# Optimization experiments

Hardware: AMD Instinct MI355X
Metric: run time of the kernel (lower is better)

Reference implementation:

```python
import jax, jax.numpy as jnp
import numpy as np

B, N, DIM, H, DH = 2, 1024, 1024, 16, 64
ROT = 32          # rotary dims (applied to first ROT channels of q,k,v)
NUM_MEM = 2       # learned memory kv
TOPK = 64         # sparse topk
QK_SCALE = 10.0   # qk_norm_scale
MASK_VAL = -jnp.finfo(jnp.float32).max


def rotate_half(x):
    # '... (2 d) -> ... 2 d', then cat(-x2, x1)
    x = x.reshape(*x.shape[:-1], 2, x.shape[-1] // 2)
    x1, x2 = x[..., 0, :], x[..., 1, :]
    return jnp.concatenate((-x2, x1), axis=-1)


def apply_rotary(t, freqs):
    # t: [b,h,n,rot], freqs: [n,rot]
    f = freqs[-t.shape[-2]:, :]
    return t * jnp.cos(f) + rotate_half(t) * jnp.sin(f)


def l2norm(t, eps=1e-12):
    n = jnp.sqrt(jnp.sum(t * t, axis=-1, keepdims=True))
    return t / jnp.maximum(n, eps)


def setup_inputs() -> dict:
    key = jax.random.key(0)
    ks = jax.random.split(key, 10)
    s = 0.02
    return {
        'x': jax.random.normal(ks[0], (B, N, DIM), jnp.float32),
        'rotary_pos_emb': jax.random.uniform(ks[1], (N, ROT), jnp.float32),
        'Wq': jax.random.normal(ks[2], (DIM, H * DH), jnp.float32) * s,
        'Wk': jax.random.normal(ks[3], (DIM, H * DH), jnp.float32) * s,
        'Wv': jax.random.normal(ks[4], (DIM, H * DH), jnp.float32) * s,
        'Wo': jax.random.normal(ks[5], (H * DH, DIM), jnp.float32) * s,
        'mem_k': jax.random.normal(ks[6], (H, NUM_MEM, DH), jnp.float32),
        'mem_v': jax.random.normal(ks[7], (H, NUM_MEM, DH), jnp.float32),
        'th_pre': jax.random.normal(ks[8], (H, H), jnp.float32) * (1.0 / H),
        'th_post': jax.random.normal(ks[9], (H, H), jnp.float32) * (1.0 / H),
    }


def reference(x, rotary_pos_emb, Wq, Wk, Wv, Wo, mem_k, mem_v, th_pre, th_post):
    b, n, _ = x.shape
    # projections -> [b,h,n,d]
    def split_heads(t):
        return t.reshape(b, n, H, DH).transpose(0, 2, 1, 3)
    q = split_heads(x @ Wq)
    k = split_heads(x @ Wk)
    v = split_heads(x @ Wv)
    # rotary on first ROT channels of q, k AND v (faithful to source)
    def rot(t):
        return jnp.concatenate(
            (apply_rotary(t[..., :ROT], rotary_pos_emb), t[..., ROT:]), axis=-1)
    q, k, v = rot(q), rot(k), rot(v)
    # memory key/values prepended along j
    mk = jnp.broadcast_to(mem_k[None], (b, H, NUM_MEM, DH))
    mv = jnp.broadcast_to(mem_v[None], (b, H, NUM_MEM, DH))
    k = jnp.concatenate((mk, k), axis=2)
    v = jnp.concatenate((mv, v), axis=2)
    # qk l2 norm (groups=1) and fixed scale
    q, k = l2norm(q), l2norm(k)
    dots = jnp.einsum('bhid,bhjd->bhij', q, k) * QK_SCALE  # [b,h,n,n+mem]
    pre_softmax_attn = dots
    # pre-softmax talking heads (1x1 conv over head dim)
    dots = jnp.einsum('hg,bgij->bhij', th_pre, dots)
    # causal mask (mem kv always visible: mask padded False on left)
    j = n + NUM_MEM
    i_idx = jnp.arange(n)[:, None]
    j_idx = jnp.arange(j)[None, :]
    causal = (j_idx - NUM_MEM) > i_idx
    dots = jnp.where(causal[None, None], MASK_VAL, dots)
    # sparse topk pruning
    top, _ = jax.lax.top_k(dots, TOPK)
    vk = top[..., -1:]
    dots = jnp.where(dots < vk, MASK_VAL, dots)
    attn = jax.nn.softmax(dots, axis=-1)
    post_softmax_attn = attn
    # post-softmax talking heads
    attn = jnp.einsum('hg,bgij->bhij', th_post, attn)
    out = jnp.einsum('bhij,bhjd->bhid', attn, v)
    out = out.transpose(0, 2, 1, 3).reshape(b, n, H * DH)
    out = out @ Wo
    return out, pre_softmax_attn, post_softmax_attn
```

## Files before the change

### kernel.cpp

```cpp
#include <hip/hip_runtime.h>
#include <stdint.h>

#define HN 16
#define DHD 64
#define NSEQ 1024
#define JCOL 1026
#define JP 1056
#define JP2 1088
#define ROTD 32
#define MASKV -3.402823466e+38f

typedef unsigned short ushort_t;
typedef __attribute__((ext_vector_type(8))) short short8;
typedef __attribute__((ext_vector_type(4))) short short4v;
typedef __attribute__((ext_vector_type(4))) float f32x4;
typedef __attribute__((ext_vector_type(2))) float f32x2;

__device__ inline ushort_t f2b(float f){ union{float f; unsigned int i;} v; v.f=f; unsigned x=v.i;
  return (ushort_t)((x + 0x7FFFu + ((x>>16)&1u))>>16); }

__device__ inline void gld16(const void* g, void* l){
  __builtin_amdgcn_global_load_lds((const __attribute__((address_space(1))) void*)g,
                                   (__attribute__((address_space(3))) void*)l, 16, 0, 0);
}

__device__ inline unsigned key_of(float f){
  unsigned u = __float_as_uint(f);
  return (u & 0x80000000u) ? ~u : (u | 0x80000000u);
}
__device__ inline float val_of(unsigned k){
  unsigned u = (k & 0x80000000u) ? (k & 0x7FFFFFFFu) : ~k;
  return __uint_as_float(u);
}

__global__ void k_zero(uint4* p, int n4){
  int i = blockIdx.x*blockDim.x + threadIdx.x;
  if (i < n4) p[i] = make_uint4(0u,0u,0u,0u);
}

__global__ __launch_bounds__(256) void k_x2b(const float4* __restrict__ x, ushort_t* __restrict__ xb){
  int i = blockIdx.x*blockDim.x + threadIdx.x;
  float4 v = x[i];
  ushort_t* d = xb + (size_t)i*4;
  d[0]=f2b(v.x); d[1]=f2b(v.y); d[2]=f2b(v.z); d[3]=f2b(v.w);
}

__global__ __launch_bounds__(256) void k_transpose(const float* w0, const float* w1,
                                                   const float* w2, const float* w3,
                                                   ushort_t* outw){
  const float* src = blockIdx.z==0?w0: blockIdx.z==1?w1: blockIdx.z==2?w2: w3;
  ushort_t* dst = outw + (size_t)blockIdx.z*1024*1024;
  __shared__ float t[64][65];
  int tid = threadIdx.x;
  int bx = blockIdx.x*64, by = blockIdx.y*64;
  #pragma unroll
  for (int p=0;p<16;p++){
    int idx = tid + p*256; int r = idx>>6, c = idx&63;
    t[r][c] = src[(size_t)(by + r)*1024 + bx + c];
  }
  __syncthreads();
  #pragma unroll
  for (int p=0;p<16;p++){
    int idx = tid + p*256; int a = idx>>6, c2 = idx&63;
    dst[(size_t)(bx + a)*1024 + by + c2] = f2b(t[c2][a]);
  }
}

__global__ __launch_bounds__(256) void k_qkv(const ushort_t* __restrict__ xb,
                                             const ushort_t* __restrict__ wt,
                                             const float* __restrict__ rpe,
                                             ushort_t* __restrict__ Qn,
                                             ushort_t* __restrict__ Kn,
                                             ushort_t* __restrict__ Vt){
  __shared__ __attribute__((aligned(16))) ushort_t As[64*32];
  __shared__ __attribute__((aligned(16))) ushort_t Bs[64*32];
  int tid = threadIdx.x;
  int m0 = blockIdx.x*64;
  int nt = blockIdx.y;
  const ushort_t* wsel = wt + (size_t)(nt>>4)*1024*1024;
  int c0 = (nt&15)*64;
  int w = tid>>6, lane = tid&63, n15 = lane&15, quad = lane>>4;
  int r = tid>>2, seg = tid&3;
  f32x4 acc[4];
  #pragma unroll
  for (int t=0;t<4;t++) acc[t] = (f32x4){0.f,0.f,0.f,0.f};
  for (int k0=0;k0<1024;k0+=32){
    __syncthreads();
    gld16(xb   + (size_t)(m0 + r)*1024 + k0 + seg*8, (void*)(As + tid*8));
    gld16(wsel + (size_t)(c0 + r)*1024 + k0 + seg*8, (void*)(Bs + tid*8));
    __builtin_amdgcn_s_waitcnt(0);
    __syncthreads();
    short8 a = *(const short8*)(As + (w*16 + n15)*32 + quad*8);
    #pragma unroll
    for (int t=0;t<4;t++){
      short8 b = *(const short8*)(Bs + (t*16 + n15)*32 + quad*8);
      acc[t] = __builtin_amdgcn_mfma_f32_16x16x32_bf16(a, b, acc[t], 0,0,0);
    }
  }
  int which = nt >> 4, h = nt & 15;
  int rowbase = m0 + w*16 + quad*4;
  int b = rowbase >> 10;
  float val[4][4];
  #pragma unroll
  for (int rr=0; rr<4; rr++){
    int n = (rowbase + rr) & 1023;
    float f0 = rpe[n*ROTD + n15];
    float f1 = rpe[n*ROTD + 16 + n15];
    float c0r = __cosf(f0), s0r = __sinf(f0);
    float c1r = __cosf(f1), s1r = __sinf(f1);
    val[0][rr] = acc[0][rr]*c0r - acc[1][rr]*s0r;
    val[1][rr] = acc[1][rr]*c1r + acc[0][rr]*s1r;
    val[2][rr] = acc[2][rr];
    val[3][rr] = acc[3][rr];
  }
  if (which < 2){
    #pragma unroll
    for (int rr=0; rr<4; rr++){
      float ss = val[0][rr]*val[0][rr] + val[1][rr]*val[1][rr]
               + val[2][rr]*val[2][rr] + val[3][rr]*val[3][rr];
      #pragma unroll
      for (int off=1; off<16; off<<=1) ss += __shfl_xor(ss, off);
      float sc = 1.f / fmaxf(sqrtf(ss), 1e-12f);
      int n = (rowbase + rr) & 1023;
      if (which == 0){
        ushort_t* dst = Qn + ((size_t)(b*16+h)*NSEQ + n)*64;
        #pragma unroll
        for (int t=0;t<4;t++) dst[t*16 + n15] = f2b(val[t][rr]*sc);
      } else {
        ushort_t* dst = Kn + ((size_t)(b*16+h)*JP2 + (n+2))*64;
        #pragma unroll
        for (int t=0;t<4;t++) dst[t*16 + n15] = f2b(val[t][rr]*sc);
      }
    }
  } else {
    #pragma unroll
    for (int rr=0; rr<4; rr++){
      int n = (rowbase + rr) & 1023;
      #pragma unroll
      for (int t=0;t<4;t++){
        int d = t*16 + n15;
        Vt[((size_t)(b*16+h)*64 + d)*JP + (n+2)] = f2b(val[t][rr]);
      }
    }
  }
}

__global__ void k_mem(const float* __restrict__ mem_k, const float* __restrict__ mem_v,
                      ushort_t* __restrict__ Kn, ushort_t* __restrict__ Vt){
  int tid = threadIdx.x;
  int d = tid & 63;
  int sub = tid >> 6;
  for (int p=0; p<8; p++){
    int pp = p*4 + sub; int h = pp >> 1, m = pp & 1;
    float kv = mem_k[(h*2+m)*64 + d];
    float ss = kv*kv;
    #pragma unroll
    for (int off=1; off<64; off<<=1) ss += __shfl_xor(ss, off);
    float sc = 1.f/fmaxf(sqrtf(ss), 1e-12f);
    ushort_t kb = f2b(kv*sc);
    ushort_t vb = f2b(mem_v[(h*2+m)*64 + d]);
    for (int b=0;b<2;b++){
      Kn[((size_t)(b*16+h)*JP2 + m)*64 + d] = kb;
      Vt[((size_t)(b*16+h)*64 + d)*JP + m] = vb;
    }
  }
}

__global__ __launch_bounds__(256) void k_dots(const ushort_t* __restrict__ Qn,
        const ushort_t* __restrict__ Kn, float* __restrict__ pre){
  __shared__ __attribute__((aligned(16))) ushort_t As[64*64];
  __shared__ __attribute__((aligned(16))) ushort_t Bs[64*64];
  int tid = threadIdx.x;
  int m0 = blockIdx.x*64;
  int n0 = blockIdx.y*64;
  int bh = blockIdx.z;
  const ushort_t* A  = Qn + (size_t)bh*NSEQ*64 + (size_t)m0*64;
  const ushort_t* Bb = Kn + (size_t)bh*JP2*64 + (size_t)n0*64;
  int w = tid>>6, lane = tid&63, n15 = lane&15, quad = lane>>4;
  gld16(A  + tid*8,        (void*)(As + tid*8));
  gld16(A  + 2048 + tid*8, (void*)(As + 2048 + tid*8));
  gld16(Bb + tid*8,        (void*)(Bs + tid*8));
  gld16(Bb + 2048 + tid*8, (void*)(Bs + 2048 + tid*8));
  __builtin_amdgcn_s_waitcnt(0);
  __syncthreads();
  f32x4 acc[4];
  #pragma unroll
  for (int t=0;t<4;t++) acc[t] = (f32x4){0.f,0.f,0.f,0.f};
  #pragma unroll
  for (int kq=0;kq<2;kq++){
    short8 a = *(const short8*)(As + (w*16+n15)*64 + kq*32 + quad*8);
    #pragma unroll
    for (int t=0;t<4;t++){
      short8 b = *(const short8*)(Bs + (t*16+n15)*64 + kq*32 + quad*8);
      acc[t] = __builtin_amdgcn_mfma_f32_16x16x32_bf16(a, b, acc[t], 0,0,0);
    }
  }
  int rowbase = m0 + w*16 + quad*4;
  #pragma unroll
  for (int t=0;t<4;t++){
    #pragma unroll
    for (int rr=0;rr<4;rr++){
      int col = n0 + t*16 + n15;
      if (col < JCOL)
        pre[((size_t)bh*NSEQ + rowbase+rr)*JCOL + col] = acc[t][rr]*10.f;
    }
  }
}

__global__ __launch_bounds__(1024, 8) void k_mixsoft(const float* __restrict__ pre,
        float* __restrict__ post, ushort_t* __restrict__ AM,
        const float* __restrict__ th_pre, const float* __restrict__ th_post){
  constexpr int NCH = 5;
  __shared__ __attribute__((aligned(16))) float S[16*1280];
  int tid  = threadIdx.x;
  int lane = tid & 63, wv = tid >> 6;
  int blk = blockIdx.x;
  int b = blk >> 10, i = blk & 1023;
  int vend  = i + 3;
  int rmaxC = (vend + 255) >> 8;

  size_t rowoff = (size_t)(b*16 + wv)*NSEQ + i;
  const float* src = pre + rowoff*JCOL;
  float* Srow = S + wv*1280;
  for (int r = 0; r < rmaxC; r++)
    gld16(src + r*256 + lane*4, (void*)(Srow + r*256 + lane*4));
  __builtin_amdgcn_s_waitcnt(0);
  __syncthreads();

  int h16 = __builtin_amdgcn_readfirstlane(wv) * 16;
  float TPr[16];
  #pragma unroll
  for (int g=0; g<16; g++) TPr[g] = th_pre[h16 + g];

  unsigned kr[NCH][4];
  #pragma unroll
  for (int r=0;r<NCH;r++){ kr[r][0]=0x00800000u; kr[r][1]=0x00800000u;
                           kr[r][2]=0x00800000u; kr[r][3]=0x00800000u; }
  #pragma unroll
  for (int r=0;r<NCH;r++) if (r < rmaxC){
    int j0 = r*256 + lane*4;
    f32x4 a = (f32x4){0.f,0.f,0.f,0.f};
    #pragma unroll
    for (int g=0; g<16; g++){
      f32x4 sv = *(const f32x4*)(S + g*1280 + j0);
      a += sv * TPr[g];
    }
    #pragma unroll
    for (int c=0;c<4;c++) if (j0 + c < vend) kr[r][c] = key_of(a[c]);
  }
  __syncthreads();

  unsigned T = 0;
  for (int it=15; it>=0; --it){
    unsigned b1 = 1u << (2*it+1), b0 = 1u << (2*it);
    unsigned t3 = T|b1|b0, t2 = T|b1, t1 = T|b0;
    int c3=0, c2=0, c1=0;
    #pragma unroll
    for (int r=0;r<NCH;r++) if (r < rmaxC){
      #pragma unroll
      for (int c=0;c<4;c++){
        unsigned kk = kr[r][c];
        c3 += __popcll(__ballot(kk >= t3));
        c2 += __popcll(__ballot(kk >= t2));
        c1 += __popcll(__ballot(kk >= t1));
      }
    }
    T = (c3>=64) ? t3 : (c2>=64) ? t2 : (c1>=64) ? t1 : T;
  }
  unsigned km = 0u;
  #pragma unroll
  for (int r=0;r<NCH;r++){
    #pragma unroll
    for (int c=0;c<4;c++){ unsigned kk = kr[r][c]; km = kk > km ? kk : km; }
  }
  #pragma unroll
  for (int off=32; off>=1; off>>=1){ unsigned o = __shfl_xor(km, off); km = o > km ? o : km; }
  float mx = val_of(km);
  float s = 0.f;
  #pragma unroll
  for (int r=0;r<NCH;r++) if (r < rmaxC){
    #pragma unroll
    for (int c=0;c<4;c++){
      unsigned kk = kr[r][c];
      if (kk >= T) s += __expf(val_of(kk) - mx);
    }
  }
  #pragma unroll
  for (int off=32; off>=1; off>>=1) s += __shfl_xor(s, off);
  float inv = 1.f / s;

  float* drow = post + rowoff*JCOL;
  #pragma unroll
  for (int r=0;r<NCH;r++) if (r < rmaxC){
    int j0 = r*256 + lane*4;
    f32x4 p;
    #pragma unroll
    for (int c=0;c<4;c++){
      unsigned kk = kr[r][c];
      float ev = (kk >= T) ? __expf(val_of(kk) - mx) : 0.f;
      p[c] = ev * inv;
    }
    *(f32x4*)(Srow + j0) = p;
    if (j0 + 3 < JCOL){
      *(f32x2*)(drow + j0)     = (f32x2){p[0], p[1]};
      *(f32x2*)(drow + j0 + 2) = (f32x2){p[2], p[3]};
    } else {
      #pragma unroll
      for (int c=0;c<4;c++) if (j0 + c < JCOL) drow[j0+c] = p[c];
    }
  }
  for (int j = rmaxC*256 + lane; j < JCOL; j += 64) drow[j] = 0.f;
  __syncthreads();

  int hp = __builtin_amdgcn_readfirstlane(wv >> 1);
  int cq = __builtin_amdgcn_readfirstlane(wv & 1);
  float tq0[16], tq1[16];
  #pragma unroll
  for (int g=0; g<16; g++){
    tq0[g] = th_post[(hp*2  )*16 + g];
    tq1[g] = th_post[(hp*2+1)*16 + g];
  }
  ushort_t* am0 = AM + ((size_t)(b*16 + hp*2  )*NSEQ + i)*JP;
  ushort_t* am1 = AM + ((size_t)(b*16 + hp*2+1)*NSEQ + i)*JP;
  for (int r = cq; r < rmaxC; r += 2){
    int j0 = r*256 + lane*4;
    f32x4 a0 = (f32x4){0.f,0.f,0.f,0.f};
    f32x4 a1 = (f32x4){0.f,0.f,0.f,0.f};
    #pragma unroll
    for (int g=0; g<16; g++){
      f32x4 sv = *(const f32x4*)(S + g*1280 + j0);
      a0 += sv * tq0[g];
      a1 += sv * tq1[g];
    }
    if (j0 + 3 < JP){
      short4v v0 = (short4v){(short)f2b(a0[0]),(short)f2b(a0[1]),(short)f2b(a0[2]),(short)f2b(a0[3])};
      short4v v1 = (short4v){(short)f2b(a1[0]),(short)f2b(a1[1]),(short)f2b(a1[2]),(short)f2b(a1[3])};
      *(short4v*)(am0 + j0) = v0;
      *(short4v*)(am1 + j0) = v1;
    } else {
      #pragma unroll
      for (int c=0;c<4;c++) if (j0 + c < JP){
        am0[j0+c] = f2b(a0[c]);
        am1[j0+c] = f2b(a1[c]);
      }
    }
  }
  {
    ushort_t* amw = AM + ((size_t)(b*16 + wv)*NSEQ + i)*JP;
    for (int j = rmaxC*256 + lane; j < JP; j += 64) amw[j] = 0;
  }
}

__global__ __launch_bounds__(256) void k_pv(const ushort_t* __restrict__ AM,
        const ushort_t* __restrict__ Vt, ushort_t* __restrict__ O1){
  __shared__ __attribute__((aligned(16))) ushort_t As[64*32];
  __shared__ __attribute__((aligned(16))) ushort_t Bs[64*32];
  int tid = threadIdx.x;
  int m0 = blockIdx.x*64;
  int bh = blockIdx.y;
  const ushort_t* Ab = AM + (size_t)bh*NSEQ*JP + (size_t)m0*JP;
  const ushort_t* Bb = Vt + (size_t)bh*64*JP;
  int w=tid>>6, lane=tid&63, n15=lane&15, quad=lane>>4;
  int r=tid>>2, seg=tid&3;
  f32x4 acc[4];
  #pragma unroll
  for (int t=0;t<4;t++) acc[t] = (f32x4){0.f,0.f,0.f,0.f};
  for (int k0=0;k0<JP;k0+=32){
    __syncthreads();
    gld16(Ab + (size_t)r*JP + k0 + seg*8, (void*)(As + tid*8));
    gld16(Bb + (size_t)r*JP + k0 + seg*8, (void*)(Bs + tid*8));
    __builtin_amdgcn_s_waitcnt(0);
    __syncthreads();
    short8 a = *(const short8*)(As + (w*16+n15)*32 + quad*8);
    #pragma unroll
    for (int t=0;t<4;t++){
      short8 b = *(const short8*)(Bs + (t*16+n15)*32 + quad*8);
      acc[t] = __builtin_amdgcn_mfma_f32_16x16x32_bf16(a, b, acc[t], 0,0,0);
    }
  }
  int b_ = bh>>4, h_ = bh&15;
  int rowbase = m0 + w*16 + quad*4;
  #pragma unroll
  for (int t=0;t<4;t++)
    #pragma unroll
    for (int rr=0;rr<4;rr++)
      O1[((size_t)b_*NSEQ + rowbase+rr)*1024 + h_*64 + t*16 + n15] = f2b(acc[t][rr]);
}

__global__ __launch_bounds__(256) void k_outproj(const ushort_t* __restrict__ o1,
        const ushort_t* __restrict__ wot, float* __restrict__ outp){
  __shared__ __attribute__((aligned(16))) ushort_t As[64*32];
  __shared__ __attribute__((aligned(16))) ushort_t Bs[64*32];
  int tid = threadIdx.x;
  int m0 = blockIdx.x*64;
  int n0 = blockIdx.y*64;
  int w = tid>>6, lane = tid&63, n15 = lane&15, quad = lane>>4;
  int r = tid>>2, seg = tid&3;
  f32x4 acc[4];
  #pragma unroll
  for (int t=0;t<4;t++) acc[t] = (f32x4){0.f,0.f,0.f,0.f};
  for (int k0=0;k0<1024;k0+=32){
    __syncthreads();
    gld16(o1  + (size_t)(m0 + r)*1024 + k0 + seg*8, (void*)(As + tid*8));
    gld16(wot + (size_t)(n0 + r)*1024 + k0 + seg*8, (void*)(Bs + tid*8));
    __builtin_amdgcn_s_waitcnt(0);
    __syncthreads();
    short8 a = *(const short8*)(As + (w*16 + n15)*32 + quad*8);
    #pragma unroll
    for (int t=0;t<4;t++){
      short8 b = *(const short8*)(Bs + (t*16 + n15)*32 + quad*8);
      acc[t] = __builtin_amdgcn_mfma_f32_16x16x32_bf16(a, b, acc[t], 0,0,0);
    }
  }
  int rowbase = m0 + w*16 + quad*4;
  #pragma unroll
  for (int t=0;t<4;t++)
    #pragma unroll
    for (int rr=0;rr<4;rr++)
      outp[(size_t)(rowbase+rr)*1024 + n0 + t*16 + n15] = acc[t][rr];
}

extern "C" void kernel_launch(void* const* d_in, const int* in_sizes, int n_in,
                              void* d_out, int out_size, void* d_ws, size_t ws_size,
                              hipStream_t stream){
  const float* x   = (const float*)d_in[0];
  const float* rpe = (const float*)d_in[1];
  const float* Wq  = (const float*)d_in[2];
  const float* Wk  = (const float*)d_in[3];
  const float* Wv  = (const float*)d_in[4];
  const float* Wo  = (const float*)d_in[5];
  const float* mk  = (const float*)d_in[6];
  const float* mv  = (const float*)d_in[7];
  const float* thp = (const float*)d_in[8];
  const float* thq = (const float*)d_in[9];
  char* ws = (char*)d_ws;
  ushort_t* AM = (ushort_t*)(ws + 0);
  ushort_t* Qn = (ushort_t*)(ws + 69206016);
  ushort_t* Kn = (ushort_t*)(ws + 73400320);
  ushort_t* Vt = (ushort_t*)(ws + 77856768);
  ushort_t* O1 = (ushort_t*)(ws + 82182144);
  ushort_t* WT = (ushort_t*)(ws + 86376448);
  ushort_t* Xb = (ushort_t*)(ws + 94765056);
  float* out0 = (float*)d_out;
  float* pre  = out0 + 2097152;
  float* post = pre + 33619968;

  k_zero<<<2144, 256, 0, stream>>>((uint4*)Kn, 548864);
  k_x2b<<<2048, 256, 0, stream>>>((const float4*)x, Xb);
  k_transpose<<<dim3(16,16,4), 256, 0, stream>>>(Wq, Wk, Wv, Wo, WT);
  k_qkv<<<dim3(32,48), 256, 0, stream>>>(Xb, WT, rpe, Qn, Kn, Vt);
  k_mem<<<1, 256, 0, stream>>>(mk, mv, Kn, Vt);
  k_dots<<<dim3(16,17,32), 256, 0, stream>>>(Qn, Kn, pre);
  k_mixsoft<<<2048, 1024, 0, stream>>>(pre, post, AM, thp, thq);
  k_pv<<<dim3(16,32), 256, 0, stream>>>(AM, Vt, O1);
  k_outproj<<<dim3(32,16), 256, 0, stream>>>(O1, WT + 3*1048576, out0);
}
```

Baseline: 544.7 us.

## Enlarge GEMM M-tiles, use DPP reductions and bitwise radix select in top-k softmax

The QKV and output-projection GEMMs now compute 128-row tiles per block, with two MFMA row-groups per wave, so each loaded weight tile is reused twice and half as many blocks are launched. In the mix/softmax kernel, the 2-bit-per-step ballot-based top-k threshold search becomes a 1-bit-per-step count reduced with DPP, and it exits early once exactly 64 keys pass. The max and sum reductions also use DPP, and exp values are cached in registers so they are not recomputed. The risks are lower occupancy and fewer blocks for the GEMMs, and up to twice as many select iterations when the early exit does not trigger.

```diff
diff --git a/kernel.cpp b/kernel.cpp
--- a/kernel.cpp
+++ b/kernel.cpp
@@ -33,6 +33,36 @@
   return __uint_as_float(u);
 }
 
+__device__ inline int dpp_add_i(int x){
+  x += __builtin_amdgcn_update_dpp(0, x, 0x111, 0xf, 0xf, true);
+  x += __builtin_amdgcn_update_dpp(0, x, 0x112, 0xf, 0xf, true);
+  x += __builtin_amdgcn_update_dpp(0, x, 0x114, 0xf, 0xf, true);
+  x += __builtin_amdgcn_update_dpp(0, x, 0x118, 0xf, 0xf, true);
+  x += __builtin_amdgcn_update_dpp(0, x, 0x142, 0xa, 0xf, true);
+  x += __builtin_amdgcn_update_dpp(0, x, 0x143, 0xc, 0xf, true);
+  return __builtin_amdgcn_readlane(x, 63);
+}
+__device__ inline float dpp_add_f(float x){
+  int xi;
+  xi = __builtin_amdgcn_update_dpp(0, __float_as_int(x), 0x111, 0xf, 0xf, true); x += __int_as_float(xi);
+  xi = __builtin_amdgcn_update_dpp(0, __float_as_int(x), 0x112, 0xf, 0xf, true); x += __int_as_float(xi);
+  xi = __builtin_amdgcn_update_dpp(0, __float_as_int(x), 0x114, 0xf, 0xf, true); x += __int_as_float(xi);
+  xi = __builtin_amdgcn_update_dpp(0, __float_as_int(x), 0x118, 0xf, 0xf, true); x += __int_as_float(xi);
+  xi = __builtin_amdgcn_update_dpp(0, __float_as_int(x), 0x142, 0xa, 0xf, true); x += __int_as_float(xi);
+  xi = __builtin_amdgcn_update_dpp(0, __float_as_int(x), 0x143, 0xc, 0xf, true); x += __int_as_float(xi);
+  return __int_as_float(__builtin_amdgcn_readlane(__float_as_int(x), 63));
+}
+__device__ inline unsigned dpp_max_u(unsigned x){
+  unsigned t;
+  t = (unsigned)__builtin_amdgcn_update_dpp(0, (int)x, 0x111, 0xf, 0xf, true); x = x > t ? x : t;
+  t = (unsigned)__builtin_amdgcn_update_dpp(0, (int)x, 0x112, 0xf, 0xf, true); x = x > t ? x : t;
+  t = (unsigned)__builtin_amdgcn_update_dpp(0, (int)x, 0x114, 0xf, 0xf, true); x = x > t ? x : t;
+  t = (unsigned)__builtin_amdgcn_update_dpp(0, (int)x, 0x118, 0xf, 0xf, true); x = x > t ? x : t;
+  t = (unsigned)__builtin_amdgcn_update_dpp(0, (int)x, 0x142, 0xa, 0xf, true); x = x > t ? x : t;
+  t = (unsigned)__builtin_amdgcn_update_dpp(0, (int)x, 0x143, 0xc, 0xf, true); x = x > t ? x : t;
+  return (unsigned)__builtin_amdgcn_readlane((int)x, 63);
+}
+
 __global__ void k_zero(uint4* p, int n4){
   int i = blockIdx.x*blockDim.x + threadIdx.x;
   if (i < n4) p[i] = make_uint4(0u,0u,0u,0u);
@@ -72,74 +102,83 @@
                                              ushort_t* __restrict__ Qn,
                                              ushort_t* __restrict__ Kn,
                                              ushort_t* __restrict__ Vt){
-  __shared__ __attribute__((aligned(16))) ushort_t As[64*32];
+  __shared__ __attribute__((aligned(16))) ushort_t As[128*32];
   __shared__ __attribute__((aligned(16))) ushort_t Bs[64*32];
   int tid = threadIdx.x;
-  int m0 = blockIdx.x*64;
+  int m0 = blockIdx.x*128;
   int nt = blockIdx.y;
   const ushort_t* wsel = wt + (size_t)(nt>>4)*1024*1024;
   int c0 = (nt&15)*64;
   int w = tid>>6, lane = tid&63, n15 = lane&15, quad = lane>>4;
   int r = tid>>2, seg = tid&3;
-  f32x4 acc[4];
-  #pragma unroll
-  for (int t=0;t<4;t++) acc[t] = (f32x4){0.f,0.f,0.f,0.f};
+  f32x4 acc[2][4];
+  #pragma unroll
+  for (int m=0;m<2;m++)
+    #pragma unroll
+    for (int t=0;t<4;t++) acc[m][t] = (f32x4){0.f,0.f,0.f,0.f};
   for (int k0=0;k0<1024;k0+=32){
     __syncthreads();
-    gld16(xb   + (size_t)(m0 + r)*1024 + k0 + seg*8, (void*)(As + tid*8));
-    gld16(wsel + (size_t)(c0 + r)*1024 + k0 + seg*8, (void*)(Bs + tid*8));
+    gld16(xb   + (size_t)(m0 + r)*1024 + k0 + seg*8,      (void*)(As + tid*8));
+    gld16(xb   + (size_t)(m0 + 64 + r)*1024 + k0 + seg*8, (void*)(As + 2048 + tid*8));
+    gld16(wsel + (size_t)(c0 + r)*1024 + k0 + seg*8,      (void*)(Bs + tid*8));
     __builtin_amdgcn_s_waitcnt(0);
     __syncthreads();
-    short8 a = *(const short8*)(As + (w*16 + n15)*32 + quad*8);
-    #pragma unroll
-    for (int t=0;t<4;t++){
-      short8 b = *(const short8*)(Bs + (t*16 + n15)*32 + quad*8);
-      acc[t] = __builtin_amdgcn_mfma_f32_16x16x32_bf16(a, b, acc[t], 0,0,0);
+    #pragma unroll
+    for (int m=0;m<2;m++){
+      short8 a = *(const short8*)(As + (w*32 + m*16 + n15)*32 + quad*8);
+      #pragma unroll
+      for (int t=0;t<4;t++){
+        short8 b = *(const short8*)(Bs + (t*16 + n15)*32 + quad*8);
+        acc[m][t] = __builtin_amdgcn_mfma_f32_16x16x32_bf16(a, b, acc[m][t], 0,0,0);
+      }
     }
   }
   int which = nt >> 4, h = nt & 15;
-  int rowbase = m0 + w*16 + quad*4;
-  int b = rowbase >> 10;
-  float val[4][4];
-  #pragma unroll
-  for (int rr=0; rr<4; rr++){
-    int n = (rowbase + rr) & 1023;
-    float f0 = rpe[n*ROTD + n15];
-    float f1 = rpe[n*ROTD + 16 + n15];
-    float c0r = __cosf(f0), s0r = __sinf(f0);
-    float c1r = __cosf(f1), s1r = __sinf(f1);
-    val[0][rr] = acc[0][rr]*c0r - acc[1][rr]*s0r;
-    val[1][rr] = acc[1][rr]*c1r + acc[0][rr]*s1r;
-    val[2][rr] = acc[2][rr];
-    val[3][rr] = acc[3][rr];
-  }
-  if (which < 2){
-    #pragma unroll
-    for (int rr=0; rr<4; rr++){
-      float ss = val[0][rr]*val[0][rr] + val[1][rr]*val[1][rr]
-               + val[2][rr]*val[2][rr] + val[3][rr]*val[3][rr];
-      #pragma unroll
-      for (int off=1; off<16; off<<=1) ss += __shfl_xor(ss, off);
-      float sc = 1.f / fmaxf(sqrtf(ss), 1e-12f);
-      int n = (rowbase + rr) & 1023;
-      if (which == 0){
-        ushort_t* dst = Qn + ((size_t)(b*16+h)*NSEQ + n)*64;
-        #pragma unroll
-        for (int t=0;t<4;t++) dst[t*16 + n15] = f2b(val[t][rr]*sc);
-      } else {
-        ushort_t* dst = Kn + ((size_t)(b*16+h)*JP2 + (n+2))*64;
-        #pragma unroll
-        for (int t=0;t<4;t++) dst[t*16 + n15] = f2b(val[t][rr]*sc);
-      }
-    }
-  } else {
+  #pragma unroll
+  for (int m=0;m<2;m++){
+    int rowbase = m0 + w*32 + m*16 + quad*4;
+    int b = rowbase >> 10;
+    float val[4][4];
     #pragma unroll
     for (int rr=0; rr<4; rr++){
       int n = (rowbase + rr) & 1023;
-      #pragma unroll
-      for (int t=0;t<4;t++){
-        int d = t*16 + n15;
-        Vt[((size_t)(b*16+h)*64 + d)*JP + (n+2)] = f2b(val[t][rr]);
+      float f0 = rpe[n*ROTD + n15];
+      float f1 = rpe[n*ROTD + 16 + n15];
+      float c0r = __cosf(f0), s0r = __sinf(f0);
+      float c1r = __cosf(f1), s1r = __sinf(f1);
+      val[0][rr] = acc[m][0][rr]*c0r - acc[m][1][rr]*s0r;
+      val[1][rr] = acc[m][1][rr]*c1r + acc[m][0][rr]*s1r;
+      val[2][rr] = acc[m][2][rr];
+      val[3][rr] = acc[m][3][rr];
+    }
+    if (which < 2){
+      #pragma unroll
+      for (int rr=0; rr<4; rr++){
+        float ss = val[0][rr]*val[0][rr] + val[1][rr]*val[1][rr]
+                 + val[2][rr]*val[2][rr] + val[3][rr]*val[3][rr];
+        #pragma unroll
+        for (int off=1; off<16; off<<=1) ss += __shfl_xor(ss, off);
+        float sc = 1.f / fmaxf(sqrtf(ss), 1e-12f);
+        int n = (rowbase + rr) & 1023;
+        if (which == 0){
+          ushort_t* dst = Qn + ((size_t)(b*16+h)*NSEQ + n)*64;
+          #pragma unroll
+          for (int t=0;t<4;t++) dst[t*16 + n15] = f2b(val[t][rr]*sc);
+        } else {
+          ushort_t* dst = Kn + ((size_t)(b*16+h)*JP2 + (n+2))*64;
+          #pragma unroll
+          for (int t=0;t<4;t++) dst[t*16 + n15] = f2b(val[t][rr]*sc);
+        }
+      }
+    } else {
+      #pragma unroll
+      for (int rr=0; rr<4; rr++){
+        int n = (rowbase + rr) & 1023;
+        #pragma unroll
+        for (int t=0;t<4;t++){
+          int d = t*16 + n15;
+          Vt[((size_t)(b*16+h)*64 + d)*JP + (n+2)] = f2b(val[t][rr]);
+        }
       }
     }
   }
@@ -251,21 +290,19 @@
   __syncthreads();
 
   unsigned T = 0;
-  for (int it=15; it>=0; --it){
-    unsigned b1 = 1u << (2*it+1), b0 = 1u << (2*it);
-    unsigned t3 = T|b1|b0, t2 = T|b1, t1 = T|b0;
-    int c3=0, c2=0, c1=0;
+  for (int bit=31; bit>=0; --bit){
+    unsigned cand = T | (1u << bit);
+    int lc = 0;
     #pragma unroll
     for (int r=0;r<NCH;r++) if (r < rmaxC){
       #pragma unroll
-      for (int c=0;c<4;c++){
-        unsigned kk = kr[r][c];
-        c3 += __popcll(__ballot(kk >= t3));
-        c2 += __popcll(__ballot(kk >= t2));
-        c1 += __popcll(__ballot(kk >= t1));
-      }
-    }
-    T = (c3>=64) ? t3 : (c2>=64) ? t2 : (c1>=64) ? t1 : T;
+      for (int c=0;c<4;c++) lc += (kr[r][c] >= cand) ? 1 : 0;
+    }
+    int tot = dpp_add_i(lc);
+    if (tot >= 64){
+      T = cand;
+      if (tot == 64) break;
+    }
   }
   unsigned km = 0u;
   #pragma unroll
@@ -273,8 +310,7 @@
     #pragma unroll
     for (int c=0;c<4;c++){ unsigned kk = kr[r][c]; km = kk > km ? kk : km; }
   }
-  #pragma unroll
-  for (int off=32; off>=1; off>>=1){ unsigned o = __shfl_xor(km, off); km = o > km ? o : km; }
+  km = dpp_max_u(km);
   float mx = val_of(km);
   float s = 0.f;
   #pragma unroll
@@ -282,11 +318,12 @@
     #pragma unroll
     for (int c=0;c<4;c++){
       unsigned kk = kr[r][c];
-      if (kk >= T) s += __expf(val_of(kk) - mx);
-    }
-  }
-  #pragma unroll
-  for (int off=32; off>=1; off>>=1) s += __shfl_xor(s, off);
+      float ev = (kk >= T) ? __expf(val_of(kk) - mx) : 0.f;
+      s += ev;
+      kr[r][c] = __float_as_uint(ev);
+    }
+  }
+  s = dpp_add_f(s);
   float inv = 1.f / s;
 
   float* drow = post + rowoff*JCOL;
@@ -295,11 +332,7 @@
     int j0 = r*256 + lane*4;
     f32x4 p;
     #pragma unroll
-    for (int c=0;c<4;c++){
-      unsigned kk = kr[r][c];
-      float ev = (kk >= T) ? __expf(val_of(kk) - mx) : 0.f;
-      p[c] = ev * inv;
-    }
+    for (int c=0;c<4;c++) p[c] = __uint_as_float(kr[r][c]) * inv;
     *(f32x4*)(Srow + j0) = p;
     if (j0 + 3 < JCOL){
       *(f32x2*)(drow + j0)     = (f32x2){p[0], p[1]};
@@ -389,35 +422,44 @@
 
 __global__ __launch_bounds__(256) void k_outproj(const ushort_t* __restrict__ o1,
         const ushort_t* __restrict__ wot, float* __restrict__ outp){
-  __shared__ __attribute__((aligned(16))) ushort_t As[64*32];
+  __shared__ __attribute__((aligned(16))) ushort_t As[128*32];
   __shared__ __attribute__((aligned(16))) ushort_t Bs[64*32];
   int tid = threadIdx.x;
-  int m0 = blockIdx.x*64;
+  int m0 = blockIdx.x*128;
   int n0 = blockIdx.y*64;
   int w = tid>>6, lane = tid&63, n15 = lane&15, quad = lane>>4;
   int r = tid>>2, seg = tid&3;
-  f32x4 acc[4];
-  #pragma unroll
-  for (int t=0;t<4;t++) acc[t] = (f32x4){0.f,0.f,0.f,0.f};
+  f32x4 acc[2][4];
+  #pragma unroll
+  for (int m=0;m<2;m++)
+    #pragma unroll
+    for (int t=0;t<4;t++) acc[m][t] = (f32x4){0.f,0.f,0.f,0.f};
   for (int k0=0;k0<1024;k0+=32){
     __syncthreads();
-    gld16(o1  + (size_t)(m0 + r)*1024 + k0 + seg*8, (void*)(As + tid*8));
-    gld16(wot + (size_t)(n0 + r)*1024 + k0 + seg*8, (void*)(Bs + tid*8));
+    gld16(o1  + (size_t)(m0 + r)*1024 + k0 + seg*8,      (void*)(As + tid*8));
+    gld16(o1  + (size_t)(m0 + 64 + r)*1024 + k0 + seg*8, (void*)(As + 2048 + tid*8));
+    gld16(wot + (size_t)(n0 + r)*1024 + k0 + seg*8,      (void*)(Bs + tid*8));
     __builtin_amdgcn_s_waitcnt(0);
     __syncthreads();
-    short8 a = *(const short8*)(As + (w*16 + n15)*32 + quad*8);
-    #pragma unroll
-    for (int t=0;t<4;t++){
-      short8 b = *(const short8*)(Bs + (t*16 + n15)*32 + quad*8);
-      acc[t] = __builtin_amdgcn_mfma_f32_16x16x32_bf16(a, b, acc[t], 0,0,0);
-    }
-  }
-  int rowbase = m0 + w*16 + quad*4;
-  #pragma unroll
-  for (int t=0;t<4;t++)
-    #pragma unroll
-    for (int rr=0;rr<4;rr++)
-      outp[(size_t)(rowbase+rr)*1024 + n0 + t*16 + n15] = acc[t][rr];
+    #pragma unroll
+    for (int m=0;m<2;m++){
+      short8 a = *(const short8*)(As + (w*32 + m*16 + n15)*32 + quad*8);
+      #pragma unroll
+      for (int t=0;t<4;t++){
+        short8 b = *(const short8*)(Bs + (t*16 + n15)*32 + quad*8);
+        acc[m][t] = __builtin_amdgcn_mfma_f32_16x16x32_bf16(a, b, acc[m][t], 0,0,0);
+      }
+    }
+  }
+  #pragma unroll
+  for (int m=0;m<2;m++){
+    int rowbase = m0 + w*32 + m*16 + quad*4;
+    #pragma unroll
+    for (int t=0;t<4;t++)
+      #pragma unroll
+      for (int rr=0;rr<4;rr++)
+        outp[(size_t)(rowbase+rr)*1024 + n0 + t*16 + n15] = acc[m][t][rr];
+  }
 }
 
 extern "C" void kernel_launch(void* const* d_in, const int* in_sizes, int n_in,
@@ -448,10 +490,10 @@
   k_zero<<<2144, 256, 0, stream>>>((uint4*)Kn, 548864);
   k_x2b<<<2048, 256, 0, stream>>>((const float4*)x, Xb);
   k_transpose<<<dim3(16,16,4), 256, 0, stream>>>(Wq, Wk, Wv, Wo, WT);
-  k_qkv<<<dim3(32,48), 256, 0, stream>>>(Xb, WT, rpe, Qn, Kn, Vt);
+  k_qkv<<<dim3(16,48), 256, 0, stream>>>(Xb, WT, rpe, Qn, Kn, Vt);
   k_mem<<<1, 256, 0, stream>>>(mk, mv, Kn, Vt);
   k_dots<<<dim3(16,17,32), 256, 0, stream>>>(Qn, Kn, pre);
   k_mixsoft<<<2048, 1024, 0, stream>>>(pre, post, AM, thp, thq);
   k_pv<<<dim3(16,32), 256, 0, stream>>>(AM, Vt, O1);
-  k_outproj<<<dim3(32,16), 256, 0, stream>>>(O1, WT + 3*1048576, out0);
-}
+  k_outproj<<<dim3(16,16), 256, 0, stream>>>(O1, WT + 3*1048576, out0);
+}
```

Result: faster. 497.2 us (-8.7%).
